# Kernel tuning notes

Measured on AMD Instinct MI355X. Metric: run time of the kernel, lower is better.

## Reference

```python
import jax, jax.numpy as jnp
import numpy as np

B, S, D, H, FF = 4, 1024, 1024, 16, 4096
HD = D // H
SCALE = float(np.sqrt(HD))
LAMBDA_MIN = 0.5
LAMBDA_MAX = 0.5
EPS = 1e-5


def _layernorm(x, g, b):
    mu = jnp.mean(x, axis=-1, keepdims=True)
    var = jnp.mean(jnp.square(x - mu), axis=-1, keepdims=True)
    return (x - mu) * jax.lax.rsqrt(var + EPS) * g + b


def _qbnn_layer(h, W, bW, J, lam_base, g, be):
    # s_prev = tanh(h); h_tilde = h W + b; delta_j = (sum_i s_prev_i J_ij) * tanh(h_tilde)_j
    s_prev = jnp.tanh(h)
    h_tilde = h @ W + bW
    s_raw = jnp.tanh(h_tilde)
    delta = (s_prev @ J) * s_raw
    lam_n = jax.nn.sigmoid(lam_base)
    dynamic_factor = 0.5  # eval mode, call_count=0 -> 0.5+0.5*sin(0)
    lam_eff = LAMBDA_MIN + (LAMBDA_MAX - LAMBDA_MIN) * (lam_n * 0.7 + dynamic_factor * 0.3)
    h_hat = h_tilde + lam_eff * delta
    return jax.nn.gelu(_layernorm(h_hat, g, be), approximate=False)


def setup_inputs() -> dict:
    key = jax.random.key(0)
    ks = jax.random.split(key, 24)
    f32 = jnp.float32
    lin = lambda k, i, o: jax.random.normal(k, (i, o), f32) / np.sqrt(i)
    inp = {
        'x': jax.random.normal(ks[0], (B, S, D), f32),
        # attention projections (stored as [in, out]; y = x @ W + b)
        'wq': lin(ks[1], D, D), 'bq': jnp.zeros((D,), f32),
        'wk': lin(ks[2], D, D), 'bk': jnp.zeros((D,), f32),
        'wv': lin(ks[3], D, D), 'bv': jnp.zeros((D,), f32),
        'wo': lin(ks[4], D, D), 'bo': jnp.zeros((D,), f32),
        'J_attn': jax.random.normal(ks[5], (H, HD, HD), f32) * 0.02,
        'lambda_attn': jnp.asarray(0.5, f32),
        'g_attn': jnp.ones((D,), f32), 'b_attn': jnp.zeros((D,), f32),
        # ffn layer 1 (D -> FF)
        'W1': lin(ks[6], D, FF), 'b1': jnp.zeros((FF,), f32),
        'J1': jax.random.normal(ks[7], (D, FF), f32) * 0.02,
        'lam1': jnp.asarray(0.5, f32),
        'g1': jnp.ones((FF,), f32), 'be1': jnp.zeros((FF,), f32),
        # ffn layer 2 (FF -> D)
        'W2': lin(ks[8], FF, D), 'b2': jnp.zeros((D,), f32),
        'J2': jax.random.normal(ks[9], (FF, D), f32) * 0.02,
        'lam2': jnp.asarray(0.5, f32),
        'g2': jnp.ones((D,), f32), 'be2': jnp.zeros((D,), f32),
        # ffn pre-norm
        'g_ffn': jnp.ones((D,), f32), 'b_ffn': jnp.zeros((D,), f32),
    }
    return inp


def reference(x, wq, bq, wk, bk, wv, bv, wo, bo, J_attn, lambda_attn, g_attn, b_attn,
              W1, b1, J1, lam1, g1, be1, W2, b2, J2, lam2, g2, be2, g_ffn, b_ffn):
    # --- attention (pre-norm) ---
    xn = _layernorm(x, g_attn, b_attn)
    split = lambda t: t.reshape(B, S, H, HD).transpose(0, 2, 1, 3)  # bshd -> bhsd
    Q = split(xn @ wq + bq)
    K = split(xn @ wk + bk)
    V = split(xn @ wv + bv)
    scores = jnp.einsum('bhid,bhjd->bhij', Q, K) / SCALE
    tQJ = jnp.einsum('bhid,hde->bhie', jnp.tanh(Q), J_attn)
    delta = jnp.einsum('bhie,bhje->bhij', tQJ, jnp.tanh(K))
    probs = jax.nn.softmax(scores + lambda_attn * delta, axis=-1)
    attn = jnp.einsum('bhij,bhjd->bhid', probs, V)
    attn = attn.transpose(0, 2, 1, 3).reshape(B, S, D) @ wo + bo
    x = x + attn
    # --- QBNN FFN (pre-norm) ---
    h = _layernorm(x, g_ffn, b_ffn)
    h = _qbnn_layer(h, W1, b1, J1, lam1, g1, be1)
    h = _qbnn_layer(h, W2, b2, J2, lam2, g2, be2)
    return x + h
```

## Files before the change

### kernel.cpp

```cpp
#include <hip/hip_runtime.h>
#include <cmath>

typedef unsigned short u16;
typedef unsigned int   u32;
typedef short bhalf8 __attribute__((ext_vector_type(8)));
typedef float fx4    __attribute__((ext_vector_type(4)));

#define B_   4
#define S_   1024
#define D_   1024
#define H_   16
#define HD_  64
#define FF_  4096
#define NTOK (B_*S_)
#define QKVW 3072

__device__ __forceinline__ float b2f(u16 u) {
    u32 x = ((u32)u) << 16;
    return __uint_as_float(x);
}
__device__ __forceinline__ u16 f2b(float f) {
    u32 u = __float_as_uint(f);
    u32 r = (u + 0x7fffu + ((u >> 16) & 1u)) >> 16;
    return (u16)r;
}

#define GLDS16(g, l) __builtin_amdgcn_global_load_lds( \
    (const __attribute__((address_space(1))) void*)(g), \
    (__attribute__((address_space(3))) void*)(l), 16, 0, 0)

__device__ __forceinline__ void tile_swz(int gx, int gy, int& bx, int& by) {
    int bid = blockIdx.x;
    int nwg = gx * gy;
    if (((nwg | gy) & 7) == 0) {
        int chunk = nwg >> 3;
        int wg = (bid & 7) * chunk + (bid >> 3);
        int tps = gx << 3;
        int sup = wg / tps, rem = wg % tps;
        bx = rem >> 3;
        by = (sup << 3) + (rem & 7);
    } else {
        bx = bid % gx; by = bid / gx;
    }
}

__global__ __launch_bounds__(256) void cvt_t_k(const float* __restrict__ w0, const float* __restrict__ w1,
                                               const float* __restrict__ w2, const float* __restrict__ w3,
                                               const float* __restrict__ W1p, const float* __restrict__ J1p,
                                               const float* __restrict__ W2p, const float* __restrict__ J2p,
                                               u16* __restrict__ dst) {
    __shared__ u16 L[64][65];
    int bid = blockIdx.x, tid = threadIdx.x;
    const float* src; size_t dbase; int Kd, Nd, tk, tn;
    if (bid < 1024)      { int m = bid >> 8, t = bid & 255;
                           src = m == 0 ? w0 : m == 1 ? w1 : m == 2 ? w2 : w3;
                           dbase = (size_t)m << 20; Kd = 1024; Nd = 1024; tk = t >> 4; tn = t & 15; }
    else if (bid < 2048) { int t = bid - 1024; src = W1p; dbase = (size_t)4  << 20; Kd = 1024; Nd = 4096; tk = t >> 6; tn = t & 63; }
    else if (bid < 3072) { int t = bid - 2048; src = J1p; dbase = (size_t)8  << 20; Kd = 1024; Nd = 4096; tk = t >> 6; tn = t & 63; }
    else if (bid < 4096) { int t = bid - 3072; src = W2p; dbase = (size_t)12 << 20; Kd = 4096; Nd = 1024; tk = t >> 4; tn = t & 15; }
    else                 { int t = bid - 4096; src = J2p; dbase = (size_t)16 << 20; Kd = 4096; Nd = 1024; tk = t >> 4; tn = t & 15; }
    int k0 = tk * 64, n0 = tn * 64;
    int r = tid >> 2, c4 = (tid & 3) * 16;
    #pragma unroll
    for (int p = 0; p < 4; ++p) {
        float4 v = *(const float4*)&src[(size_t)(k0 + r) * Nd + n0 + c4 + p * 4];
        L[r][c4 + p * 4 + 0] = f2b(v.x);
        L[r][c4 + p * 4 + 1] = f2b(v.y);
        L[r][c4 + p * 4 + 2] = f2b(v.z);
        L[r][c4 + p * 4 + 3] = f2b(v.w);
    }
    __syncthreads();
    u16 o[16];
    #pragma unroll
    for (int j = 0; j < 16; ++j) o[j] = L[c4 + j][r];
    *(uint4*)&dst[dbase + (size_t)(n0 + r) * Kd + k0 + c4]     = *(uint4*)&o[0];
    *(uint4*)&dst[dbase + (size_t)(n0 + r) * Kd + k0 + c4 + 8] = *(uint4*)&o[8];
}

__global__ __launch_bounds__(256) void tanh_k(const u16* __restrict__ in, u16* __restrict__ outb) {
    size_t idx = ((size_t)blockIdx.x * 256 + threadIdx.x) * 8;
    uint4 v = *(const uint4*)&in[idx];
    const u16* p = (const u16*)&v;
    u16 o[8];
    #pragma unroll
    for (int j = 0; j < 8; ++j) o[j] = f2b(tanhf(b2f(p[j])));
    *(uint4*)&outb[idx] = *(uint4*)o;
}

template <int EPI, bool SEG>
__global__ __launch_bounds__(256, 2) void gemm128(const u16* __restrict__ A,
                                                  const u16* __restrict__ Bt,
                                                  const float* __restrict__ bA,
                                                  const float* __restrict__ bB,
                                                  const float* __restrict__ bC,
                                                  const float* __restrict__ resid,
                                                  void* __restrict__ Cout,
                                                  int M, int N, int K) {
    __shared__ u16 As[128 * 32];
    __shared__ u16 Bs[128 * 32];
    const int tid = threadIdx.x;
    const int w = tid >> 6, ln = tid & 63;
    const int q = ln >> 4, mr = ln & 15;
    int bx, by;
    tile_swz(N >> 7, M >> 7, bx, by);
    const int m0 = by * 128, n0 = bx * 128;
    const int wm = (w >> 1) * 64, wn = (w & 1) * 64;
    const int sr = w * 16 + (ln >> 2);
    const int sc = ((ln & 3) ^ ((ln >> 3) & 3)) * 8;
    const int qx = (q ^ ((mr >> 1) & 3)) * 8;

    fx4 acc[4][4];
    #pragma unroll
    for (int i = 0; i < 4; ++i)
        #pragma unroll
        for (int j = 0; j < 4; ++j) acc[i][j] = (fx4){0.f, 0.f, 0.f, 0.f};

    const u16* Ab0 = A  + (size_t)(m0 + sr) * K + sc;
    const u16* Ab1 = A  + (size_t)(m0 + sr + 64) * K + sc;
    const u16* Bb0 = Bt + (size_t)(n0 + sr) * K + sc;
    const u16* Bb1 = Bt + (size_t)(n0 + sr + 64) * K + sc;

    for (int k0 = 0; k0 < K; k0 += 32) {
        __syncthreads();
        GLDS16(Ab0 + k0, &As[w * 512]);
        GLDS16(Ab1 + k0, &As[(w + 4) * 512]);
        GLDS16(Bb0 + k0, &Bs[w * 512]);
        GLDS16(Bb1 + k0, &Bs[(w + 4) * 512]);
        __syncthreads();

        bhalf8 af[4], bf[4];
        #pragma unroll
        for (int i = 0; i < 4; ++i) af[i] = *(const bhalf8*)&As[(wm + i * 16 + mr) * 32 + qx];
        #pragma unroll
        for (int j = 0; j < 4; ++j) bf[j] = *(const bhalf8*)&Bs[(wn + j * 16 + mr) * 32 + qx];
        #pragma unroll
        for (int i = 0; i < 4; ++i)
            #pragma unroll
            for (int j = 0; j < 4; ++j)
                acc[i][j] = __builtin_amdgcn_mfma_f32_16x16x32_bf16(af[i], bf[j], acc[i][j], 0, 0, 0);
    }

    #pragma unroll
    for (int j = 0; j < 4; ++j) {
        int col = n0 + wn + j * 16 + mr;
        float bs;
        if (SEG) {
            const float* bp = col < 1024 ? bA : (col < 2048 ? bB : bC);
            bs = bp[col & 1023];
        } else {
            bs = bA ? bA[col] : 0.f;
        }
        #pragma unroll
        for (int i = 0; i < 4; ++i) {
            #pragma unroll
            for (int r = 0; r < 4; ++r) {
                int row    = m0 + wm + i * 16 + q * 4 + r;
                size_t idx = (size_t)row * N + col;
                float v    = acc[i][j][r] + bs;
                if (EPI == 0) {
                    ((u16*)Cout)[idx] = f2b(v);
                } else if (EPI == 1) {
                    ((float*)Cout)[idx] = v + resid[idx];
                } else {
                    float ht = b2f(((u16*)Cout)[idx]);
                    ((u16*)Cout)[idx] = f2b(ht + 0.5f * v * tanhf(ht));
                }
            }
        }
    }
}

__global__ __launch_bounds__(256, 2) void dgemm128(const u16* __restrict__ A,
                                                   const u16* __restrict__ At,
                                                   const u16* __restrict__ WT,
                                                   const u16* __restrict__ JT,
                                                   const float* __restrict__ bias,
                                                   u16* __restrict__ Cout,
                                                   int M, int N, int K) {
    __shared__ u16 As[2][128 * 32];
    __shared__ u16 Ts[2][128 * 32];
    __shared__ u16 Ws[2][128 * 32];
    __shared__ u16 Js[2][128 * 32];
    const int tid = threadIdx.x;
    const int w = tid >> 6, ln = tid & 63;
    const int q = ln >> 4, mr = ln & 15;
    int bx, by;
    tile_swz(N >> 7, M >> 7, bx, by);
    const int m0 = by * 128, n0 = bx * 128;
    const int wm = (w >> 1) * 64, wn = (w & 1) * 64;
    const int sr = w * 16 + (ln >> 2);
    const int sc = ((ln & 3) ^ ((ln >> 3) & 3)) * 8;
    const int qx = (q ^ ((mr >> 1) & 3)) * 8;

    fx4 aw[4][4], aj[4][4];
    #pragma unroll
    for (int i = 0; i < 4; ++i)
        #pragma unroll
        for (int j = 0; j < 4; ++j) {
            aw[i][j] = (fx4){0.f, 0.f, 0.f, 0.f};
            aj[i][j] = (fx4){0.f, 0.f, 0.f, 0.f};
        }

    const u16* Ab0 = A  + (size_t)(m0 + sr) * K + sc;
    const u16* Ab1 = A  + (size_t)(m0 + sr + 64) * K + sc;
    const u16* Tb0 = At + (size_t)(m0 + sr) * K + sc;
    const u16* Tb1 = At + (size_t)(m0 + sr + 64) * K + sc;
    const u16* Wb0 = WT + (size_t)(n0 + sr) * K + sc;
    const u16* Wb1 = WT + (size_t)(n0 + sr + 64) * K + sc;
    const u16* Jb0 = JT + (size_t)(n0 + sr) * K + sc;
    const u16* Jb1 = JT + (size_t)(n0 + sr + 64) * K + sc;

#define DG_STAGE(pp, kk) do { \
        GLDS16(Ab0 + (kk), &As[pp][w * 512]); \
        GLDS16(Ab1 + (kk), &As[pp][(w + 4) * 512]); \
        GLDS16(Tb0 + (kk), &Ts[pp][w * 512]); \
        GLDS16(Tb1 + (kk), &Ts[pp][(w + 4) * 512]); \
        GLDS16(Wb0 + (kk), &Ws[pp][w * 512]); \
        GLDS16(Wb1 + (kk), &Ws[pp][(w + 4) * 512]); \
        GLDS16(Jb0 + (kk), &Js[pp][w * 512]); \
        GLDS16(Jb1 + (kk), &Js[pp][(w + 4) * 512]); \
    } while (0)

    const int NT = K >> 5;
    DG_STAGE(0, 0);
    int p = 0;
    for (int t = 0; t < NT; ++t) {
        if (t + 1 < NT) {
            DG_STAGE(p ^ 1, (t + 1) << 5);
            asm volatile("s_waitcnt vmcnt(8)" ::: "memory");
        } else {
            asm volatile("s_waitcnt vmcnt(0)" ::: "memory");
        }
        __builtin_amdgcn_s_barrier();

        bhalf8 af[4], tf[4];
        #pragma unroll
        for (int i = 0; i < 4; ++i) {
            af[i] = *(const bhalf8*)&As[p][(wm + i * 16 + mr) * 32 + qx];
            tf[i] = *(const bhalf8*)&Ts[p][(wm + i * 16 + mr) * 32 + qx];
        }
        __builtin_amdgcn_s_setprio(1);
        #pragma unroll
        for (int j = 0; j < 4; ++j) {
            bhalf8 wf = *(const bhalf8*)&Ws[p][(wn + j * 16 + mr) * 32 + qx];
            bhalf8 jf = *(const bhalf8*)&Js[p][(wn + j * 16 + mr) * 32 + qx];
            #pragma unroll
            for (int i = 0; i < 4; ++i) {
                aw[i][j] = __builtin_amdgcn_mfma_f32_16x16x32_bf16(af[i], wf, aw[i][j], 0, 0, 0);
                aj[i][j] = __builtin_amdgcn_mfma_f32_16x16x32_bf16(tf[i], jf, aj[i][j], 0, 0, 0);
            }
        }
        __builtin_amdgcn_s_setprio(0);
        asm volatile("s_waitcnt lgkmcnt(0)" ::: "memory");
        __builtin_amdgcn_s_barrier();
        p ^= 1;
    }
#undef DG_STAGE

    #pragma unroll
    for (int j = 0; j < 4; ++j) {
        int col = n0 + wn + j * 16 + mr;
        float bs = bias[col];
        #pragma unroll
        for (int i = 0; i < 4; ++i) {
            #pragma unroll
            for (int r = 0; r < 4; ++r) {
                int row    = m0 + wm + i * 16 + q * 4 + r;
                size_t idx = (size_t)row * N + col;
                float ht   = aw[i][j][r] + bs;
                Cout[idx]  = f2b(ht + 0.5f * aj[i][j][r] * tanhf(ht));
            }
        }
    }
}

__global__ __launch_bounds__(256) void ln_k(const float* __restrict__ xin,
                                            const float* __restrict__ g,
                                            const float* __restrict__ bb,
                                            u16* __restrict__ out, int W) {
    __shared__ float red[8], red2[8], stats[2];
    int row = blockIdx.x, tid = threadIdx.x;
    float s = 0.f, ss = 0.f;
    for (int c = tid; c < W; c += 256) {
        float v = xin[(size_t)row * W + c];
        s += v; ss += v * v;
    }
    #pragma unroll
    for (int off = 32; off; off >>= 1) { s += __shfl_xor(s, off); ss += __shfl_xor(ss, off); }
    int wave = tid >> 6, lane = tid & 63;
    if (lane == 0) { red[wave] = s; red2[wave] = ss; }
    __syncthreads();
    if (tid == 0) {
        float S = 0.f, SS = 0.f;
        for (int w2 = 0; w2 < 4; ++w2) { S += red[w2]; SS += red2[w2]; }
        float mu = S / W;
        stats[0] = mu;
        stats[1] = rsqrtf(SS / W - mu * mu + 1e-5f);
    }
    __syncthreads();
    float mu = stats[0], rs = stats[1];
    for (int c = tid; c < W; c += 256)
        out[(size_t)row * W + c] = f2b((xin[(size_t)row * W + c] - mu) * rs * g[c] + bb[c]);
}

template <bool RES, bool OUT_F32>
__global__ __launch_bounds__(256) void lngelu_k(const u16* __restrict__ u,
                                                const float* __restrict__ g,
                                                const float* __restrict__ be,
                                                const float* __restrict__ resid,
                                                void* __restrict__ out, int W) {
    __shared__ float ub[4096];
    __shared__ float red[8], red2[8], stats[2];
    int row = blockIdx.x, tid = threadIdx.x;
    float s = 0.f, ss = 0.f;
    for (int c = tid; c < W; c += 256) {
        float v = b2f(u[(size_t)row * W + c]);
        ub[c] = v; s += v; ss += v * v;
    }
    #pragma unroll
    for (int off = 32; off; off >>= 1) { s += __shfl_xor(s, off); ss += __shfl_xor(ss, off); }
    int wave = tid >> 6, lane = tid & 63;
    if (lane == 0) { red[wave] = s; red2[wave] = ss; }
    __syncthreads();
    if (tid == 0) {
        float S = 0.f, SS = 0.f;
        for (int w2 = 0; w2 < 4; ++w2) { S += red[w2]; SS += red2[w2]; }
        float mu = S / W;
        stats[0] = mu;
        stats[1] = rsqrtf(SS / W - mu * mu + 1e-5f);
    }
    __syncthreads();
    float mu = stats[0], rs = stats[1];
    for (int c = tid; c < W; c += 256) {
        float v = (ub[c] - mu) * rs * g[c] + be[c];
        float y = 0.5f * v * (1.f + erff(v * 0.70710678118654752f));
        if (RES) y += resid[(size_t)row * W + c];
        if (OUT_F32) ((float*)out)[(size_t)row * W + c] = y;
        else         ((u16*)out)[(size_t)row * W + c] = f2b(y);
    }
}

__global__ __launch_bounds__(256) void aug_q_k(const u16* __restrict__ QKV,
                                               const float* __restrict__ J,
                                               const float* __restrict__ lamp,
                                               u16* __restrict__ QA) {
    __shared__ float Jl[64][68];
    __shared__ float Tq[64][65];
    int blk = blockIdx.x;
    int bh = blk >> 4, st = blk & 15;
    int b = bh >> 4, h = bh & 15;
    int s0 = st * 64;
    int tid = threadIdx.x;
    float lam = lamp[0];

    for (int i = tid; i < 4096; i += 256)
        Jl[i >> 6][i & 63] = J[h * 4096 + i];
    for (int i = tid; i < 4096; i += 256) {
        int r = i >> 6, c = i & 63;
        float v  = b2f(QKV[(size_t)(b * S_ + s0 + r) * QKVW + h * 64 + c]);
        Tq[r][c] = tanhf(v);
        QA[((size_t)(bh * S_ + s0 + r)) * 128 + c] = f2b(v * 0.125f);
    }
    __syncthreads();

    int r = tid >> 2, c0 = (tid & 3) * 16;
    float acc[16];
    #pragma unroll
    for (int j = 0; j < 16; ++j) acc[j] = 0.f;
    for (int k = 0; k < 64; ++k) {
        float a = Tq[r][k];
        #pragma unroll
        for (int j4 = 0; j4 < 4; ++j4) {
            float4 jv = *(const float4*)&Jl[k][c0 + j4 * 4];
            acc[j4 * 4 + 0] += a * jv.x;
            acc[j4 * 4 + 1] += a * jv.y;
            acc[j4 * 4 + 2] += a * jv.z;
            acc[j4 * 4 + 3] += a * jv.w;
        }
    }
    size_t orow = ((size_t)(bh * S_ + s0 + r)) * 128 + 64 + c0;
    #pragma unroll
    for (int j = 0; j < 16; ++j) QA[orow + j] = f2b(lam * acc[j]);
}

__global__ __launch_bounds__(256) void aug_k_k(const u16* __restrict__ QKV,
                                               u16* __restrict__ KA) {
    int idx = blockIdx.x * 256 + threadIdx.x;
    int d = idx & (D_ - 1);
    int bs = idx >> 10;
    int h = d >> 6, hd = d & 63;
    int b = bs >> 10, si = bs & (S_ - 1);
    u16 v      = QKV[(size_t)bs * QKVW + 1024 + d];
    size_t row = (size_t)((b * H_ + h) * S_ + si);
    KA[row * 128 + hd]      = v;
    KA[row * 128 + 64 + hd] = f2b(tanhf(b2f(v)));
}

#define QS_STRIDE 136
#define PS_STRIDE 72
__global__ __launch_bounds__(256) void attn_k(const u16* __restrict__ QA,
                                              const u16* __restrict__ KA,
                                              const u16* __restrict__ QKV,
                                              u16* __restrict__ out) {
    __shared__ u16 Qs[64 * QS_STRIDE];
    __shared__ u16 Ks[64 * QS_STRIDE];
    __shared__ u16 Vt[64 * PS_STRIDE];
    __shared__ u16 Ps[4 * 16 * PS_STRIDE];

    const int tid  = threadIdx.x;
    const int w    = tid >> 6, lane = tid & 63;
    const int q    = lane >> 4, mr = lane & 15;
    const int bh   = blockIdx.x >> 4;
    const int qt   = blockIdx.x & 15;
    const int b    = bh >> 4, h = bh & 15;

    #pragma unroll
    for (int p = 0; p < 4; ++p) {
        int idx = p * 2048 + tid * 8;
        int row = idx >> 7, col = idx & 127;
        uint4 v4 = *(const uint4*)&QA[((size_t)(bh * S_ + qt * 64 + row)) * 128 + col];
        *(uint4*)&Qs[row * QS_STRIDE + col] = v4;
    }

    fx4 zero = {0.f, 0.f, 0.f, 0.f};
    fx4 O[4] = {zero, zero, zero, zero};
    float m[4]  = {-3e38f, -3e38f, -3e38f, -3e38f};
    float l[4]  = {0.f, 0.f, 0.f, 0.f};

    for (int kt = 0; kt < 16; ++kt) {
        #pragma unroll
        for (int p = 0; p < 4; ++p) {
            int idx = p * 2048 + tid * 8;
            int row = idx >> 7, col = idx & 127;
            uint4 v4 = *(const uint4*)&KA[((size_t)(bh * S_ + kt * 64 + row)) * 128 + col];
            *(uint4*)&Ks[row * QS_STRIDE + col] = v4;
        }
        #pragma unroll
        for (int p = 0; p < 2; ++p) {
            int idx = p * 2048 + tid * 8;
            int key = idx >> 6, d0 = idx & 63;
            uint4 v4 = *(const uint4*)&QKV[((size_t)(b * S_ + kt * 64 + key)) * QKVW + 2048 + h * 64 + d0];
            const u16* vp = (const u16*)&v4;
            #pragma unroll
            for (int j = 0; j < 8; ++j) Vt[(d0 + j) * PS_STRIDE + key] = vp[j];
        }
        __syncthreads();

        fx4 St[4] = {zero, zero, zero, zero};
        bhalf8 afr[4];
        #pragma unroll
        for (int ks = 0; ks < 4; ++ks)
            afr[ks] = *(const bhalf8*)&Qs[(w * 16 + mr) * QS_STRIDE + ks * 32 + q * 8];
        __builtin_amdgcn_s_setprio(1);
        #pragma unroll
        for (int nt = 0; nt < 4; ++nt) {
            #pragma unroll
            for (int ks = 0; ks < 4; ++ks) {
                bhalf8 bf = *(const bhalf8*)&Ks[(nt * 16 + mr) * QS_STRIDE + ks * 32 + q * 8];
                St[nt] = __builtin_amdgcn_mfma_f32_16x16x32_bf16(afr[ks], bf, St[nt], 0, 0, 0);
            }
        }
        __builtin_amdgcn_s_setprio(0);

        float alpha[4];
        #pragma unroll
        for (int r = 0; r < 4; ++r) {
            float mx = fmaxf(fmaxf(St[0][r], St[1][r]), fmaxf(St[2][r], St[3][r]));
            #pragma unroll
            for (int off = 8; off; off >>= 1) mx = fmaxf(mx, __shfl_xor(mx, off));
            float nm = fmaxf(m[r], mx);
            alpha[r] = __expf(m[r] - nm);
            m[r] = nm;
            float ps = 0.f;
            #pragma unroll
            for (int nt = 0; nt < 4; ++nt) {
                float p = __expf(St[nt][r] - nm);
                St[nt][r] = p;
                ps += p;
            }
            #pragma unroll
            for (int off = 8; off; off >>= 1) ps += __shfl_xor(ps, off);
            l[r] = l[r] * alpha[r] + ps;
        }
        #pragma unroll
        for (int nt = 0; nt < 4; ++nt) {
            #pragma unroll
            for (int r = 0; r < 4; ++r) {
                Ps[(w * 16 + q * 4 + r) * PS_STRIDE + nt * 16 + mr] = f2b(St[nt][r]);
                O[nt][r] *= alpha[r];
            }
        }

        __builtin_amdgcn_s_setprio(1);
        #pragma unroll
        for (int ks = 0; ks < 2; ++ks) {
            bhalf8 pa = *(const bhalf8*)&Ps[(w * 16 + mr) * PS_STRIDE + ks * 32 + q * 8];
            #pragma unroll
            for (int nt = 0; nt < 4; ++nt) {
                bhalf8 bf = *(const bhalf8*)&Vt[(nt * 16 + mr) * PS_STRIDE + ks * 32 + q * 8];
                O[nt] = __builtin_amdgcn_mfma_f32_16x16x32_bf16(pa, bf, O[nt], 0, 0, 0);
            }
        }
        __builtin_amdgcn_s_setprio(0);
        __syncthreads();
    }

    #pragma unroll
    for (int nt = 0; nt < 4; ++nt) {
        int d = nt * 16 + mr;
        #pragma unroll
        for (int r = 0; r < 4; ++r) {
            int row = qt * 64 + w * 16 + q * 4 + r;
            out[((size_t)(b * S_ + row)) * D_ + h * 64 + d] = f2b(O[nt][r] / l[r]);
        }
    }
}

extern "C" void kernel_launch(void* const* d_in, const int* in_sizes, int n_in,
                              void* d_out, int out_size, void* d_ws, size_t ws_size,
                              hipStream_t stream) {
    const float* x      = (const float*)d_in[0];
    const float* wq     = (const float*)d_in[1];
    const float* bq     = (const float*)d_in[2];
    const float* wk     = (const float*)d_in[3];
    const float* bk     = (const float*)d_in[4];
    const float* wv     = (const float*)d_in[5];
    const float* bv     = (const float*)d_in[6];
    const float* wo     = (const float*)d_in[7];
    const float* bo     = (const float*)d_in[8];
    const float* Jattn  = (const float*)d_in[9];
    const float* lamA   = (const float*)d_in[10];
    const float* g_attn = (const float*)d_in[11];
    const float* b_attn = (const float*)d_in[12];
    const float* W1     = (const float*)d_in[13];
    const float* b1     = (const float*)d_in[14];
    const float* J1     = (const float*)d_in[15];
    const float* g1     = (const float*)d_in[17];
    const float* be1    = (const float*)d_in[18];
    const float* W2     = (const float*)d_in[19];
    const float* b2     = (const float*)d_in[20];
    const float* J2     = (const float*)d_in[21];
    const float* g2     = (const float*)d_in[23];
    const float* be2    = (const float*)d_in[24];
    const float* g_ffn  = (const float*)d_in[25];
    const float* b_ffn  = (const float*)d_in[26];
    float* out = (float*)d_out;
    (void)in_sizes; (void)n_in; (void)out_size;

    char* wsp = (char*)d_ws;
    const size_t MB = 1u << 20;
    u16* WB = (u16*)(wsp);
    const u16* qkvT = WB;
    const u16* woT  = WB + ((size_t)3 << 20);
    const u16* W1T  = WB + ((size_t)4 << 20);
    const u16* J1T  = WB + ((size_t)8 << 20);
    const u16* W2T  = WB + ((size_t)12 << 20);
    const u16* J2T  = WB + ((size_t)16 << 20);
    u16*   XN   = (u16*)(wsp + 40 * MB);
    u16*   AT   = (u16*)(wsp + 40 * MB);
    u16*   Ht1  = (u16*)(wsp + 40 * MB);
    u16*   U2   = (u16*)(wsp + 40 * MB);
    u16*   QKVb = (u16*)(wsp + 48 * MB);
    u16*   Hb   = (u16*)(wsp + 48 * MB);
    float* X2   = (float*)(wsp + 56 * MB);
    u16*   QA   = (u16*)(wsp + 72 * MB);
    u16*   KA   = (u16*)(wsp + 88 * MB);
    u16*   U1   = (u16*)(wsp + 72 * MB);
    u16*   Ht2  = (u16*)(wsp + 104 * MB);
    const bool dual2 = ws_size >= 136 * MB;

    dim3 blk(256);
    cvt_t_k<<<5120, blk, 0, stream>>>(wq, wk, wv, wo, W1, J1, W2, J2, WB);
    ln_k<<<NTOK, blk, 0, stream>>>(x, g_attn, b_attn, XN, D_);
    gemm128<0, true><<<(QKVW / 128) * (NTOK / 128), blk, 0, stream>>>(XN, qkvT, bq, bk, bv, nullptr, QKVb, NTOK, QKVW, D_);
    aug_q_k<<<B_ * H_ * (S_ / 64), blk, 0, stream>>>(QKVb, Jattn, lamA, QA);
    aug_k_k<<<(NTOK * D_) / 256, blk, 0, stream>>>(QKVb, KA);
    attn_k<<<B_ * H_ * (S_ / 64), blk, 0, stream>>>(QA, KA, QKVb, AT);
    gemm128<1, false><<<(D_ / 128) * (NTOK / 128), blk, 0, stream>>>(AT, woT, bo, nullptr, nullptr, x, X2, NTOK, D_, D_);
    ln_k<<<NTOK, blk, 0, stream>>>(X2, g_ffn, b_ffn, Hb, D_);
    tanh_k<<<(NTOK * D_) / 2048, blk, 0, stream>>>(Hb, Ht1);
    dgemm128<<<(FF_ / 128) * (NTOK / 128), blk, 0, stream>>>(Hb, Ht1, W1T, J1T, b1, U1, NTOK, FF_, D_);
    lngelu_k<false, false><<<NTOK, blk, 0, stream>>>(U1, g1, be1, nullptr, U1, FF_);
    if (dual2) {
        tanh_k<<<(NTOK * FF_) / 2048, blk, 0, stream>>>(U1, Ht2);
        dgemm128<<<(D_ / 128) * (NTOK / 128), blk, 0, stream>>>(U1, Ht2, W2T, J2T, b2, U2, NTOK, D_, FF_);
    } else {
        gemm128<0, false><<<(D_ / 128) * (NTOK / 128), blk, 0, stream>>>(U1, W2T, b2, nullptr, nullptr, nullptr, U2, NTOK, D_, FF_);
        tanh_k<<<(NTOK * FF_) / 2048, blk, 0, stream>>>(U1, U1);
        gemm128<2, false><<<(D_ / 128) * (NTOK / 128), blk, 0, stream>>>(U1, J2T, nullptr, nullptr, nullptr, nullptr, U2, NTOK, D_, FF_);
    }
    lngelu_k<true, true><<<NTOK, blk, 0, stream>>>(U2, g2, be2, X2, out, D_);
}
```

Measured before the change: 694.9 us.

## Replace GEMMs with templated 512-thread triple-buffered kernel and drop dual GEMM

Swaps the single-stage 256-thread gemm128 and the fused dual-accumulator dgemm128 for one templated 512-thread GEMM. It uses configurable block and warp tiles, a three-slot global-to-LDS pipeline with explicit vmcnt waits, and larger 256x256 tiles for the FF1 projection. The FFN layers now run as two sequential GEMMs, the second folding the tanh-modulated correction into its epilogue. tanhf is replaced by an exp-based fast tanh. The split adds an extra read/write pass over the output buffer that the fused dual kernel avoided.

Result: slower. 716.7 us (+3.1%).

```diff
diff --git a/kernel.cpp b/kernel.cpp
--- a/kernel.cpp
+++ b/kernel.cpp
@@ -24,10 +24,23 @@
     u32 r = (u + 0x7fffu + ((u >> 16) & 1u)) >> 16;
     return (u16)r;
 }
+__device__ __forceinline__ float ftanh(float x) {
+    float e = __expf(2.f * x);
+    return 1.f - 2.f / (e + 1.f);
+}
 
 #define GLDS16(g, l) __builtin_amdgcn_global_load_lds( \
     (const __attribute__((address_space(1))) void*)(g), \
     (__attribute__((address_space(3))) void*)(l), 16, 0, 0)
+
+template <int N> __device__ __forceinline__ void waitvm() {
+    if constexpr (N == 8) asm volatile("s_waitcnt vmcnt(8)" ::: "memory");
+    else if constexpr (N == 6) asm volatile("s_waitcnt vmcnt(6)" ::: "memory");
+    else if constexpr (N == 4) asm volatile("s_waitcnt vmcnt(4)" ::: "memory");
+    else if constexpr (N == 3) asm volatile("s_waitcnt vmcnt(3)" ::: "memory");
+    else if constexpr (N == 2) asm volatile("s_waitcnt vmcnt(2)" ::: "memory");
+    else asm volatile("s_waitcnt vmcnt(0)" ::: "memory");
+}
 
 __device__ __forceinline__ void tile_swz(int gx, int gy, int& bx, int& by) {
     int bid = blockIdx.x;
@@ -83,66 +96,107 @@
     const u16* p = (const u16*)&v;
     u16 o[8];
     #pragma unroll
-    for (int j = 0; j < 8; ++j) o[j] = f2b(tanhf(b2f(p[j])));
+    for (int j = 0; j < 8; ++j) o[j] = f2b(ftanh(b2f(p[j])));
     *(uint4*)&outb[idx] = *(uint4*)o;
 }
 
-template <int EPI, bool SEG>
-__global__ __launch_bounds__(256, 2) void gemm128(const u16* __restrict__ A,
-                                                  const u16* __restrict__ Bt,
-                                                  const float* __restrict__ bA,
-                                                  const float* __restrict__ bB,
-                                                  const float* __restrict__ bC,
-                                                  const float* __restrict__ resid,
-                                                  void* __restrict__ Cout,
-                                                  int M, int N, int K) {
-    __shared__ u16 As[128 * 32];
-    __shared__ u16 Bs[128 * 32];
+template <int BM, int BN, int WM, int WN, int EPI, bool SEG>
+__global__ __launch_bounds__(512, 2) void gemmP(const u16* __restrict__ A,
+                                                const u16* __restrict__ Bt,
+                                                const float* __restrict__ bA,
+                                                const float* __restrict__ bB,
+                                                const float* __restrict__ bC,
+                                                const float* __restrict__ resid,
+                                                void* __restrict__ Cout,
+                                                int M, int N, int K) {
+    constexpr int IA = BM / 128;
+    constexpr int IB = BN / 128;
+    constexpr int NWN = BN / WN;
+    constexpr int FM = WM / 16, FN = WN / 16;
+    __shared__ u16 As[3][BM * 32];
+    __shared__ u16 Bs[3][BN * 32];
+
     const int tid = threadIdx.x;
     const int w = tid >> 6, ln = tid & 63;
     const int q = ln >> 4, mr = ln & 15;
+    const int wmi = w / NWN, wni = w % NWN;
     int bx, by;
-    tile_swz(N >> 7, M >> 7, bx, by);
-    const int m0 = by * 128, n0 = bx * 128;
-    const int wm = (w >> 1) * 64, wn = (w & 1) * 64;
-    const int sr = w * 16 + (ln >> 2);
-    const int sc = ((ln & 3) ^ ((ln >> 3) & 3)) * 8;
-    const int qx = (q ^ ((mr >> 1) & 3)) * 8;
-
-    fx4 acc[4][4];
-    #pragma unroll
-    for (int i = 0; i < 4; ++i)
-        #pragma unroll
-        for (int j = 0; j < 4; ++j) acc[i][j] = (fx4){0.f, 0.f, 0.f, 0.f};
-
-    const u16* Ab0 = A  + (size_t)(m0 + sr) * K + sc;
-    const u16* Ab1 = A  + (size_t)(m0 + sr + 64) * K + sc;
-    const u16* Bb0 = Bt + (size_t)(n0 + sr) * K + sc;
-    const u16* Bb1 = Bt + (size_t)(n0 + sr + 64) * K + sc;
-
-    for (int k0 = 0; k0 < K; k0 += 32) {
-        __syncthreads();
-        GLDS16(Ab0 + k0, &As[w * 512]);
-        GLDS16(Ab1 + k0, &As[(w + 4) * 512]);
-        GLDS16(Bb0 + k0, &Bs[w * 512]);
-        GLDS16(Bb1 + k0, &Bs[(w + 4) * 512]);
-        __syncthreads();
-
-        bhalf8 af[4], bf[4];
-        #pragma unroll
-        for (int i = 0; i < 4; ++i) af[i] = *(const bhalf8*)&As[(wm + i * 16 + mr) * 32 + qx];
-        #pragma unroll
-        for (int j = 0; j < 4; ++j) bf[j] = *(const bhalf8*)&Bs[(wn + j * 16 + mr) * 32 + qx];
-        #pragma unroll
-        for (int i = 0; i < 4; ++i)
-            #pragma unroll
-            for (int j = 0; j < 4; ++j)
-                acc[i][j] = __builtin_amdgcn_mfma_f32_16x16x32_bf16(af[i], bf[j], acc[i][j], 0, 0, 0);
-    }
-
-    #pragma unroll
-    for (int j = 0; j < 4; ++j) {
-        int col = n0 + wn + j * 16 + mr;
+    tile_swz(N / BN, M / BM, bx, by);
+    const int m0 = by * BM, n0 = bx * BN;
+
+    const int lr = ln >> 2;
+    const int sc = 8 * ((ln & 3) ^ ((ln >> 3) & 3));
+    const int qx8 = 8 * (q ^ ((mr >> 1) & 3));
+
+    const u16* aA[IA];
+    const u16* aB[IB];
+    #pragma unroll
+    for (int i = 0; i < IA; ++i)
+        aA[i] = A + (size_t)(m0 + 16 * (w + 8 * i) + lr) * K + sc;
+    #pragma unroll
+    for (int i = 0; i < IB; ++i)
+        aB[i] = Bt + (size_t)(n0 + 16 * (w + 8 * i) + lr) * K + sc;
+
+    fx4 acc[FM][FN];
+    #pragma unroll
+    for (int i = 0; i < FM; ++i)
+        #pragma unroll
+        for (int j = 0; j < FN; ++j) acc[i][j] = (fx4){0.f, 0.f, 0.f, 0.f};
+
+#define GP_STAGE(slot, kk) do { \
+        _Pragma("unroll") \
+        for (int i = 0; i < IA; ++i) GLDS16(aA[i] + (kk), &As[slot][(16 * (w + 8 * i)) * 32]); \
+        _Pragma("unroll") \
+        for (int i = 0; i < IB; ++i) GLDS16(aB[i] + (kk), &Bs[slot][(16 * (w + 8 * i)) * 32]); \
+    } while (0)
+
+    const int NT = K >> 5;
+    GP_STAGE(0, 0);
+    GP_STAGE(1, 32);
+    int sl = 0, st = 2;
+    for (int t = 0; t < NT; ++t) {
+        if (t + 2 < NT) {
+            GP_STAGE(st, (t + 2) << 5);
+            waitvm<2 * (IA + IB)>();
+        } else if (t + 1 < NT) {
+            waitvm<IA + IB>();
+        } else {
+            waitvm<0>();
+        }
+        __builtin_amdgcn_sched_barrier(0);
+        __builtin_amdgcn_s_barrier();
+        __builtin_amdgcn_sched_barrier(0);
+
+        bhalf8 afr[FM], bfr[FN];
+        const u16* Ap = &As[sl][0];
+        const u16* Bp = &Bs[sl][0];
+        #pragma unroll
+        for (int fm = 0; fm < FM; ++fm)
+            afr[fm] = *(const bhalf8*)&Ap[(wmi * WM + fm * 16 + mr) * 32 + qx8];
+        #pragma unroll
+        for (int fn = 0; fn < FN; ++fn)
+            bfr[fn] = *(const bhalf8*)&Bp[(wni * WN + fn * 16 + mr) * 32 + qx8];
+        asm volatile("s_waitcnt lgkmcnt(0)" ::: "memory");
+        __builtin_amdgcn_sched_barrier(0);
+        __builtin_amdgcn_s_barrier();
+        __builtin_amdgcn_sched_barrier(0);
+
+        __builtin_amdgcn_s_setprio(1);
+        #pragma unroll
+        for (int fm = 0; fm < FM; ++fm)
+            #pragma unroll
+            for (int fn = 0; fn < FN; ++fn)
+                acc[fm][fn] = __builtin_amdgcn_mfma_f32_16x16x32_bf16(afr[fm], bfr[fn], acc[fm][fn], 0, 0, 0);
+        __builtin_amdgcn_s_setprio(0);
+
+        sl = sl == 2 ? 0 : sl + 1;
+        st = st == 2 ? 0 : st + 1;
+    }
+#undef GP_STAGE
+
+    #pragma unroll
+    for (int fn = 0; fn < FN; ++fn) {
+        int col = n0 + wni * WN + fn * 16 + mr;
         float bs;
         if (SEG) {
             const float* bp = col < 1024 ? bA : (col < 2048 ? bB : bC);
@@ -151,124 +205,20 @@
             bs = bA ? bA[col] : 0.f;
         }
         #pragma unroll
-        for (int i = 0; i < 4; ++i) {
+        for (int fm = 0; fm < FM; ++fm) {
             #pragma unroll
             for (int r = 0; r < 4; ++r) {
-                int row    = m0 + wm + i * 16 + q * 4 + r;
+                int row    = m0 + wmi * WM + fm * 16 + q * 4 + r;
                 size_t idx = (size_t)row * N + col;
-                float v    = acc[i][j][r] + bs;
+                float v    = acc[fm][fn][r] + bs;
                 if (EPI == 0) {
                     ((u16*)Cout)[idx] = f2b(v);
                 } else if (EPI == 1) {
                     ((float*)Cout)[idx] = v + resid[idx];
                 } else {
                     float ht = b2f(((u16*)Cout)[idx]);
-                    ((u16*)Cout)[idx] = f2b(ht + 0.5f * v * tanhf(ht));
+                    ((u16*)Cout)[idx] = f2b(ht + 0.5f * v * ftanh(ht));
                 }
-            }
-        }
-    }
-}
-
-__global__ __launch_bounds__(256, 2) void dgemm128(const u16* __restrict__ A,
-                                                   const u16* __restrict__ At,
-                                                   const u16* __restrict__ WT,
-                                                   const u16* __restrict__ JT,
-                                                   const float* __restrict__ bias,
-                                                   u16* __restrict__ Cout,
-                                                   int M, int N, int K) {
-    __shared__ u16 As[2][128 * 32];
-    __shared__ u16 Ts[2][128 * 32];
-    __shared__ u16 Ws[2][128 * 32];
-    __shared__ u16 Js[2][128 * 32];
-    const int tid = threadIdx.x;
-    const int w = tid >> 6, ln = tid & 63;
-    const int q = ln >> 4, mr = ln & 15;
-    int bx, by;
-    tile_swz(N >> 7, M >> 7, bx, by);
-    const int m0 = by * 128, n0 = bx * 128;
-    const int wm = (w >> 1) * 64, wn = (w & 1) * 64;
-    const int sr = w * 16 + (ln >> 2);
-    const int sc = ((ln & 3) ^ ((ln >> 3) & 3)) * 8;
-    const int qx = (q ^ ((mr >> 1) & 3)) * 8;
-
-    fx4 aw[4][4], aj[4][4];
-    #pragma unroll
-    for (int i = 0; i < 4; ++i)
-        #pragma unroll
-        for (int j = 0; j < 4; ++j) {
-            aw[i][j] = (fx4){0.f, 0.f, 0.f, 0.f};
-            aj[i][j] = (fx4){0.f, 0.f, 0.f, 0.f};
-        }
-
-    const u16* Ab0 = A  + (size_t)(m0 + sr) * K + sc;
-    const u16* Ab1 = A  + (size_t)(m0 + sr + 64) * K + sc;
-    const u16* Tb0 = At + (size_t)(m0 + sr) * K + sc;
-    const u16* Tb1 = At + (size_t)(m0 + sr + 64) * K + sc;
-    const u16* Wb0 = WT + (size_t)(n0 + sr) * K + sc;
-    const u16* Wb1 = WT + (size_t)(n0 + sr + 64) * K + sc;
-    const u16* Jb0 = JT + (size_t)(n0 + sr) * K + sc;
-    const u16* Jb1 = JT + (size_t)(n0 + sr + 64) * K + sc;
-
-#define DG_STAGE(pp, kk) do { \
-        GLDS16(Ab0 + (kk), &As[pp][w * 512]); \
-        GLDS16(Ab1 + (kk), &As[pp][(w + 4) * 512]); \
-        GLDS16(Tb0 + (kk), &Ts[pp][w * 512]); \
-        GLDS16(Tb1 + (kk), &Ts[pp][(w + 4) * 512]); \
-        GLDS16(Wb0 + (kk), &Ws[pp][w * 512]); \
-        GLDS16(Wb1 + (kk), &Ws[pp][(w + 4) * 512]); \
-        GLDS16(Jb0 + (kk), &Js[pp][w * 512]); \
-        GLDS16(Jb1 + (kk), &Js[pp][(w + 4) * 512]); \
-    } while (0)
-
-    const int NT = K >> 5;
-    DG_STAGE(0, 0);
-    int p = 0;
-    for (int t = 0; t < NT; ++t) {
-        if (t + 1 < NT) {
-            DG_STAGE(p ^ 1, (t + 1) << 5);
-            asm volatile("s_waitcnt vmcnt(8)" ::: "memory");
-        } else {
-            asm volatile("s_waitcnt vmcnt(0)" ::: "memory");
-        }
-        __builtin_amdgcn_s_barrier();
-
-        bhalf8 af[4], tf[4];
-        #pragma unroll
-        for (int i = 0; i < 4; ++i) {
-            af[i] = *(const bhalf8*)&As[p][(wm + i * 16 + mr) * 32 + qx];
-            tf[i] = *(const bhalf8*)&Ts[p][(wm + i * 16 + mr) * 32 + qx];
-        }
-        __builtin_amdgcn_s_setprio(1);
-        #pragma unroll
-        for (int j = 0; j < 4; ++j) {
-            bhalf8 wf = *(const bhalf8*)&Ws[p][(wn + j * 16 + mr) * 32 + qx];
-            bhalf8 jf = *(const bhalf8*)&Js[p][(wn + j * 16 + mr) * 32 + qx];
-            #pragma unroll
-            for (int i = 0; i < 4; ++i) {
-                aw[i][j] = __builtin_amdgcn_mfma_f32_16x16x32_bf16(af[i], wf, aw[i][j], 0, 0, 0);
-                aj[i][j] = __builtin_amdgcn_mfma_f32_16x16x32_bf16(tf[i], jf, aj[i][j], 0, 0, 0);
-            }
-        }
-        __builtin_amdgcn_s_setprio(0);
-        asm volatile("s_waitcnt lgkmcnt(0)" ::: "memory");
-        __builtin_amdgcn_s_barrier();
-        p ^= 1;
-    }
-#undef DG_STAGE
-
-    #pragma unroll
-    for (int j = 0; j < 4; ++j) {
-        int col = n0 + wn + j * 16 + mr;
-        float bs = bias[col];
-        #pragma unroll
-        for (int i = 0; i < 4; ++i) {
-            #pragma unroll
-            for (int r = 0; r < 4; ++r) {
-                int row    = m0 + wm + i * 16 + q * 4 + r;
-                size_t idx = (size_t)row * N + col;
-                float ht   = aw[i][j][r] + bs;
-                Cout[idx]  = f2b(ht + 0.5f * aj[i][j][r] * tanhf(ht));
             }
         }
     }
@@ -358,7 +308,7 @@
     for (int i = tid; i < 4096; i += 256) {
         int r = i >> 6, c = i & 63;
         float v  = b2f(QKV[(size_t)(b * S_ + s0 + r) * QKVW + h * 64 + c]);
-        Tq[r][c] = tanhf(v);
+        Tq[r][c] = ftanh(v);
         QA[((size_t)(bh * S_ + s0 + r)) * 128 + c] = f2b(v * 0.125f);
     }
     __syncthreads();
@@ -393,7 +343,7 @@
     u16 v      = QKV[(size_t)bs * QKVW + 1024 + d];
     size_t row = (size_t)((b * H_ + h) * S_ + si);
     KA[row * 128 + hd]      = v;
-    KA[row * 128 + 64 + hd] = f2b(tanhf(b2f(v)));
+    KA[row * 128 + 64 + hd] = f2b(ftanh(b2f(v)));
 }
 
 #define QS_STRIDE 136
@@ -545,7 +495,7 @@
     const float* g_ffn  = (const float*)d_in[25];
     const float* b_ffn  = (const float*)d_in[26];
     float* out = (float*)d_out;
-    (void)in_sizes; (void)n_in; (void)out_size;
+    (void)in_sizes; (void)n_in; (void)out_size; (void)ws_size;
 
     char* wsp = (char*)d_ws;
     const size_t MB = 1u << 20;
@@ -558,7 +508,6 @@
     const u16* J2T  = WB + ((size_t)16 << 20);
     u16*   XN   = (u16*)(wsp + 40 * MB);
     u16*   AT   = (u16*)(wsp + 40 * MB);
-    u16*   Ht1  = (u16*)(wsp + 40 * MB);
     u16*   U2   = (u16*)(wsp + 40 * MB);
     u16*   QKVb = (u16*)(wsp + 48 * MB);
     u16*   Hb   = (u16*)(wsp + 48 * MB);
@@ -566,28 +515,28 @@
     u16*   QA   = (u16*)(wsp + 72 * MB);
     u16*   KA   = (u16*)(wsp + 88 * MB);
     u16*   U1   = (u16*)(wsp + 72 * MB);
-    u16*   Ht2  = (u16*)(wsp + 104 * MB);
-    const bool dual2 = ws_size >= 136 * MB;
-
-    dim3 blk(256);
+
+    dim3 blk(256), blk5(512);
     cvt_t_k<<<5120, blk, 0, stream>>>(wq, wk, wv, wo, W1, J1, W2, J2, WB);
     ln_k<<<NTOK, blk, 0, stream>>>(x, g_attn, b_attn, XN, D_);
-    gemm128<0, true><<<(QKVW / 128) * (NTOK / 128), blk, 0, stream>>>(XN, qkvT, bq, bk, bv, nullptr, QKVb, NTOK, QKVW, D_);
+    gemmP<128, 256, 64, 64, 0, true><<<(QKVW / 256) * (NTOK / 128), blk5, 0, stream>>>(
+        XN, qkvT, bq, bk, bv, nullptr, QKVb, NTOK, QKVW, D_);
     aug_q_k<<<B_ * H_ * (S_ / 64), blk, 0, stream>>>(QKVb, Jattn, lamA, QA);
     aug_k_k<<<(NTOK * D_) / 256, blk, 0, stream>>>(QKVb, KA);
     attn_k<<<B_ * H_ * (S_ / 64), blk, 0, stream>>>(QA, KA, QKVb, AT);
-    gemm128<1, false><<<(D_ / 128) * (NTOK / 128), blk, 0, stream>>>(AT, woT, bo, nullptr, nullptr, x, X2, NTOK, D_, D_);
+    gemmP<128, 128, 64, 32, 1, false><<<(D_ / 128) * (NTOK / 128), blk5, 0, stream>>>(
+        AT, woT, bo, nullptr, nullptr, x, X2, NTOK, D_, D_);
     ln_k<<<NTOK, blk, 0, stream>>>(X2, g_ffn, b_ffn, Hb, D_);
-    tanh_k<<<(NTOK * D_) / 2048, blk, 0, stream>>>(Hb, Ht1);
-    dgemm128<<<(FF_ / 128) * (NTOK / 128), blk, 0, stream>>>(Hb, Ht1, W1T, J1T, b1, U1, NTOK, FF_, D_);
+    gemmP<256, 256, 128, 64, 0, false><<<(FF_ / 256) * (NTOK / 256), blk5, 0, stream>>>(
+        Hb, W1T, b1, nullptr, nullptr, nullptr, U1, NTOK, FF_, D_);
+    tanh_k<<<(NTOK * D_) / 2048, blk, 0, stream>>>(Hb, Hb);
+    gemmP<256, 256, 128, 64, 2, false><<<(FF_ / 256) * (NTOK / 256), blk5, 0, stream>>>(
+        Hb, J1T, nullptr, nullptr, nullptr, nullptr, U1, NTOK, FF_, D_);
     lngelu_k<false, false><<<NTOK, blk, 0, stream>>>(U1, g1, be1, nullptr, U1, FF_);
-    if (dual2) {
-        tanh_k<<<(NTOK * FF_) / 2048, blk, 0, stream>>>(U1, Ht2);
-        dgemm128<<<(D_ / 128) * (NTOK / 128), blk, 0, stream>>>(U1, Ht2, W2T, J2T, b2, U2, NTOK, D_, FF_);
-    } else {
-        gemm128<0, false><<<(D_ / 128) * (NTOK / 128), blk, 0, stream>>>(U1, W2T, b2, nullptr, nullptr, nullptr, U2, NTOK, D_, FF_);
-        tanh_k<<<(NTOK * FF_) / 2048, blk, 0, stream>>>(U1, U1);
-        gemm128<2, false><<<(D_ / 128) * (NTOK / 128), blk, 0, stream>>>(U1, J2T, nullptr, nullptr, nullptr, nullptr, U2, NTOK, D_, FF_);
-    }
+    gemmP<128, 128, 64, 32, 0, false><<<(D_ / 128) * (NTOK / 128), blk5, 0, stream>>>(
+        U1, W2T, b2, nullptr, nullptr, nullptr, U2, NTOK, D_, FF_);
+    tanh_k<<<(NTOK * FF_) / 2048, blk, 0, stream>>>(U1, U1);
+    gemmP<128, 128, 64, 32, 2, false><<<(D_ / 128) * (NTOK / 128), blk5, 0, stream>>>(
+        U1, J2T, nullptr, nullptr, nullptr, nullptr, U2, NTOK, D_, FF_);
     lngelu_k<true, true><<<NTOK, blk, 0, stream>>>(U2, g2, be2, X2, out, D_);
 }
```
